# Kernel tuning notes

Hardware: AMD Instinct MI355X
Metric: run time of the kernel (lower is better)

The kernel has to match this reference:

```python
import jax, jax.numpy as jnp
import numpy as np

N_NODES = 100000
N_EDGES = 1250000
N_GRAPHS = 512
HIDDEN = 64
F_IN = 3
N_CLASSES = 5


def setup_inputs() -> dict:
    key = jax.random.key(0)
    ks = jax.random.split(key, 8)
    x = jax.random.normal(ks[0], (N_NODES, F_IN), dtype=jnp.float32)
    edge_index = jax.random.randint(ks[1], (2, N_EDGES), 0, N_NODES, dtype=jnp.int64)
    batch = jnp.sort(jax.random.randint(ks[2], (N_NODES,), 0, N_GRAPHS, dtype=jnp.int64))
    def glorot(k, shape):
        lim = (6.0 / (shape[0] + shape[1])) ** 0.5
        return jax.random.uniform(k, shape, jnp.float32, -lim, lim)
    return {
        "x": x,
        "edge_index": edge_index,
        "batch": batch,
        "W1": glorot(ks[3], (F_IN, HIDDEN)),
        "b1": jnp.zeros((HIDDEN,), jnp.float32),
        "W2": glorot(ks[4], (HIDDEN, HIDDEN)),
        "b2": jnp.zeros((HIDDEN,), jnp.float32),
        "Wl": glorot(ks[5], (HIDDEN, N_CLASSES)),
        "bl": jnp.zeros((N_CLASSES,), jnp.float32),
    }


def _gcn_conv(x, W, b, src, dst, deg_inv_sqrt):
    # GCNConv: x' = D^{-1/2} (A + I) D^{-1/2} X W + b  (self-loops added)
    h = x @ W                                   # [N, H]
    norm = deg_inv_sqrt[src] * deg_inv_sqrt[dst]  # per-edge scale
    agg = jax.ops.segment_sum(h[src] * norm[:, None], dst, num_segments=N_NODES)
    agg = agg + h * (deg_inv_sqrt * deg_inv_sqrt)[:, None]  # self-loop term
    return agg + b


def reference(x, edge_index, batch, W1, b1, W2, b2, Wl, bl):
    src, dst = edge_index[0], edge_index[1]
    # degree (with self-loop) on destination nodes, as in PyG GCNConv
    ones = jnp.ones((N_EDGES,), jnp.float32)
    deg = jax.ops.segment_sum(ones, dst, num_segments=N_NODES) + 1.0
    deg_inv_sqrt = 1.0 / jnp.sqrt(deg)

    h = jax.nn.relu(_gcn_conv(x, W1, b1, src, dst, deg_inv_sqrt))
    h = _gcn_conv(h, W2, b2, src, dst, deg_inv_sqrt)

    # global_mean_pool over graph ids
    sums = jax.ops.segment_sum(h, batch, num_segments=N_GRAPHS)
    cnts = jax.ops.segment_sum(jnp.ones((N_NODES,), jnp.float32), batch, num_segments=N_GRAPHS)
    pooled = sums / jnp.maximum(cnts, 1.0)[:, None]

    # dropout p=0.5 is identity in eval mode
    return pooled @ Wl + bl
```

## Files before the change

### kernel.cpp

```cpp
#include <hip/hip_runtime.h>
#include <hip/hip_bf16.h>

#define N_NODES   100000
#define N_EDGES   1250000
#define N_GRAPHS  512
#define HIDDEN    64
#define F_IN      3
#define N_CLASSES 5

#define BKT_SHIFT 8
#define BKT_NODES 256
#define N_BKT     ((N_NODES + BKT_NODES - 1) / BKT_NODES)
#define CAP       4096
#define EBLK      512
#define ECHUNK    ((N_EDGES + EBLK - 1) / EBLK)
#define SCT       512
#define NREP      8

__device__ __forceinline__ unsigned short f2bf(float f) {
    unsigned u = __float_as_uint(f);
    u += 0x7FFF + ((u >> 16) & 1);
    return (unsigned short)(u >> 16);
}

__global__ void k_scat(const int* __restrict__ src, const int* __restrict__ dst,
                       const float* __restrict__ W2, const float* __restrict__ Wl,
                       const float* __restrict__ b2, const float* __restrict__ bl,
                       const int* __restrict__ batch,
                       int* __restrict__ gcur, int* __restrict__ ebuf,
                       float* __restrict__ Wc, float* __restrict__ bc,
                       int* __restrict__ gstart) {
    int b = blockIdx.x;
    int tid = threadIdx.x;
    if (b >= EBLK) {
        int bb = b - EBLK;
        if (bb == 0) {
            for (int t = tid; t < HIDDEN * N_CLASSES + N_CLASSES; t += SCT) {
                if (t < HIDDEN * N_CLASSES) {
                    int k = t / N_CLASSES, c = t % N_CLASSES;
                    float acc = 0.0f;
#pragma unroll
                    for (int j = 0; j < HIDDEN; j++)
                        acc = fmaf(W2[k * HIDDEN + j], Wl[j * N_CLASSES + c], acc);
                    Wc[t] = acc;
                } else {
                    int c = t - HIDDEN * N_CLASSES;
                    float acc = bl[c];
#pragma unroll
                    for (int j = 0; j < HIDDEN; j++)
                        acc = fmaf(b2[j], Wl[j * N_CLASSES + c], acc);
                    bc[c] = acc;
                }
            }
            return;
        }
        int n = (bb - 1) * SCT + tid;
        if (n >= N_NODES) return;
        if (n == 0) {
            for (int g = 0; g <= batch[0]; g++) gstart[g] = 0;
        } else {
            int b0 = batch[n - 1], b1 = batch[n];
            for (int g = b0 + 1; g <= b1; g++) gstart[g] = n;
        }
        if (n == N_NODES - 1) {
            for (int g = batch[n] + 1; g <= N_GRAPHS; g++) gstart[g] = N_NODES;
        }
        return;
    }
    __shared__ int pk[ECHUNK];
    __shared__ unsigned short bkl[ECHUNK];
    __shared__ int spk[ECHUNK];
    __shared__ unsigned short sbk[ECHUNK];
    __shared__ int h[N_BKT];
    __shared__ int lsc[N_BKT];
    __shared__ int gb[N_BKT];
    __shared__ int cur[N_BKT];
    for (int i = tid; i < N_BKT; i += SCT) h[i] = 0;
    __syncthreads();
    int e0 = b * ECHUNK;
    int m = min(ECHUNK, N_EDGES - e0);
    for (int i = tid; i < m; i += SCT) {
        int s = src[e0 + i], d = dst[e0 + i];
        int bk = d >> BKT_SHIFT;
        pk[i] = (s << BKT_SHIFT) | (d & (BKT_NODES - 1));
        bkl[i] = (unsigned short)bk;
        atomicAdd(&h[bk], 1);
    }
    __syncthreads();
    if (tid < N_BKT) lsc[tid] = h[tid];
    __syncthreads();
    for (int off = 1; off < N_BKT; off <<= 1) {
        int t = 0;
        if (tid < N_BKT && tid >= off) t = lsc[tid - off];
        __syncthreads();
        if (tid < N_BKT) lsc[tid] += t;
        __syncthreads();
    }
    if (tid < N_BKT) {
        gb[tid] = atomicAdd(&gcur[tid], h[tid]);
        cur[tid] = lsc[tid] - h[tid];
    }
    __syncthreads();
    for (int i = tid; i < m; i += SCT) {
        int bk = bkl[i];
        int p = atomicAdd(&cur[bk], 1);
        spk[p] = pk[i];
        sbk[p] = (unsigned short)bk;
    }
    __syncthreads();
    for (int i = tid; i < m; i += SCT) {
        int bk = sbk[i];
        int gpos = gb[bk] + (i - (lsc[bk] - h[bk]));
        if (gpos < CAP)
            ebuf[bk * CAP + gpos] = spk[i];
    }
}

__global__ void k_bktfill(const int* __restrict__ ebuf, const int* __restrict__ gcur,
                          const float* __restrict__ x,
                          int* __restrict__ rowptr, int* __restrict__ deg,
                          float* __restrict__ dis, uint2* __restrict__ xs4,
                          int* __restrict__ elist) {
    __shared__ int eb_l[CAP];
    __shared__ int sorted_l[CAP];
    __shared__ int cnt_l[BKT_NODES];
    __shared__ int cur_l[BKT_NODES];
    __shared__ int ps[BKT_NODES];
    int b = blockIdx.x, tid = threadIdx.x;
    int n0 = b * BKT_NODES;
    int e0 = b * CAP;
    int cnt = min(gcur[b], CAP);
    if (tid < BKT_NODES) cnt_l[tid] = 0;
    __syncthreads();
    for (int i = tid; i < cnt; i += 1024) {
        int pe = ebuf[e0 + i];
        eb_l[i] = pe;
        atomicAdd(&cnt_l[pe & (BKT_NODES - 1)], 1);
    }
    __syncthreads();
    if (tid < BKT_NODES) ps[tid] = cnt_l[tid];
    __syncthreads();
    for (int off = 1; off < BKT_NODES; off <<= 1) {
        int t = 0;
        if (tid < BKT_NODES && tid >= off) t = ps[tid - off];
        __syncthreads();
        if (tid < BKT_NODES) ps[tid] += t;
        __syncthreads();
    }
    if (tid < BKT_NODES) {
        int node = n0 + tid;
        int excl = ps[tid] - cnt_l[tid];
        cur_l[tid] = excl;
        if (node < N_NODES) {
            rowptr[node] = e0 + excl;
            deg[node] = cnt_l[tid];
            float dv = rsqrtf((float)cnt_l[tid] + 1.0f);
            dis[node] = dv;
            float x0 = x[node * 3 + 0], x1 = x[node * 3 + 1], x2 = x[node * 3 + 2];
            xs4[node] = make_uint2((unsigned)f2bf(x0 * dv) |
                                   ((unsigned)f2bf(x1 * dv) << 16),
                                   (unsigned)f2bf(x2 * dv));
        }
    }
    __syncthreads();
    for (int i = tid; i < cnt; i += 1024) {
        int pe = eb_l[i];
        int pos = atomicAdd(&cur_l[pe & (BKT_NODES - 1)], 1);
        sorted_l[pos] = ((unsigned)pe) >> BKT_SHIFT;
    }
    __syncthreads();
    for (int i = tid; i < cnt; i += 1024)
        elist[e0 + i] = sorted_l[i];
}

__global__ void k_l1fused(const int* __restrict__ rp, const int* __restrict__ degA,
                          const int* __restrict__ elist,
                          const float* __restrict__ dis, const uint2* __restrict__ xs4,
                          const float* __restrict__ W1, const float* __restrict__ b1,
                          unsigned* __restrict__ h1b) {
    int w = threadIdx.x >> 6, lane = threadIdx.x & 63;
    int q4 = lane >> 4;
    int j  = lane & 15;
    int node = blockIdx.x * 16 + w * 4 + q4;
    int start = rp[node], dg = degA[node];
    float a0 = 0.f, a1 = 0.f, a2 = 0.f;
    for (int k = 0; k < dg; k += 32) {
        int ia = k + j, ib = k + 16 + j;
        bool aa = ia < dg, ab = ib < dg;
        int sa = elist[start + (aa ? ia : 0)];
        int sb = elist[start + (ab ? ib : 0)];
        uint2 ua = xs4[sa];
        uint2 ub = xs4[sb];
        float ma = aa ? 1.0f : 0.0f;
        float mb = ab ? 1.0f : 0.0f;
        a0 = fmaf(__uint_as_float(ua.x << 16), ma, a0);
        a1 = fmaf(__uint_as_float(ua.x & 0xFFFF0000u), ma, a1);
        a2 = fmaf(__uint_as_float(ua.y << 16), ma, a2);
        a0 = fmaf(__uint_as_float(ub.x << 16), mb, a0);
        a1 = fmaf(__uint_as_float(ub.x & 0xFFFF0000u), mb, a1);
        a2 = fmaf(__uint_as_float(ub.y << 16), mb, a2);
    }
#pragma unroll
    for (int off = 1; off < 16; off <<= 1) {
        a0 += __shfl_xor(a0, off);
        a1 += __shfl_xor(a1, off);
        a2 += __shfl_xor(a2, off);
    }
    uint2 un = xs4[node];
    float dn = dis[node];
    a0 = dn * (a0 + __uint_as_float(un.x << 16));
    a1 = dn * (a1 + __uint_as_float(un.x & 0xFFFF0000u));
    a2 = dn * (a2 + __uint_as_float(un.y << 16));
    float v[4];
#pragma unroll
    for (int i = 0; i < 4; i++) {
        int c = 4 * j + i;
        float t = a0 * W1[c] + a1 * W1[HIDDEN + c] + a2 * W1[2 * HIDDEN + c] + b1[c];
        v[i] = fmaxf(t, 0.0f) * dn;
    }
    unsigned w0 = (unsigned)f2bf(v[0]) | ((unsigned)f2bf(v[1]) << 16);
    unsigned w1 = (unsigned)f2bf(v[2]) | ((unsigned)f2bf(v[3]) << 16);
    *(uint2*)(h1b + (size_t)node * 32 + j * 2) = make_uint2(w0, w1);
}

__global__ void k_gatherpool(const int* __restrict__ rp, const int* __restrict__ degA,
                             const int* __restrict__ elist,
                             const float* __restrict__ dis,
                             const unsigned* __restrict__ h1b,
                             const int* __restrict__ batch,
                             float* __restrict__ gsum8) {
    __shared__ float acc_s[8][HIDDEN];
    __shared__ int gid[8];
    int w = threadIdx.x >> 6, lane = threadIdx.x & 63;
    int half = lane >> 5;
    int l32 = lane & 31;
    int node = blockIdx.x * 8 + w * 2 + half;
    int start = rp[node], dg = degA[node];
    int eg = l32 >> 3;
    int ch = lane & 7;
    float acc[8] = {0.f, 0.f, 0.f, 0.f, 0.f, 0.f, 0.f, 0.f};
    for (int k = 0; k < dg; k += 16) {
        int i0 = k + eg, i1 = k + 4 + eg, i2 = k + 8 + eg, i3 = k + 12 + eg;
        bool a0b = i0 < dg, a1b = i1 < dg, a2b = i2 < dg, a3b = i3 < dg;
        int s0 = elist[start + (a0b ? i0 : 0)];
        int s1 = elist[start + (a1b ? i1 : 0)];
        int s2 = elist[start + (a2b ? i2 : 0)];
        int s3 = elist[start + (a3b ? i3 : 0)];
        float m0 = a0b ? 1.0f : 0.0f;
        float m1 = a1b ? 1.0f : 0.0f;
        float m2 = a2b ? 1.0f : 0.0f;
        float m3 = a3b ? 1.0f : 0.0f;
        uint4 u0 = *(const uint4*)(h1b + (size_t)s0 * 32 + ch * 4);
        uint4 u1 = *(const uint4*)(h1b + (size_t)s1 * 32 + ch * 4);
        uint4 u2 = *(const uint4*)(h1b + (size_t)s2 * 32 + ch * 4);
        uint4 u3 = *(const uint4*)(h1b + (size_t)s3 * 32 + ch * 4);
        acc[0] = fmaf(__uint_as_float(u0.x << 16),          m0, acc[0]);
        acc[1] = fmaf(__uint_as_float(u0.x & 0xFFFF0000u),  m0, acc[1]);
        acc[2] = fmaf(__uint_as_float(u0.y << 16),          m0, acc[2]);
        acc[3] = fmaf(__uint_as_float(u0.y & 0xFFFF0000u),  m0, acc[3]);
        acc[4] = fmaf(__uint_as_float(u0.z << 16),          m0, acc[4]);
        acc[5] = fmaf(__uint_as_float(u0.z & 0xFFFF0000u),  m0, acc[5]);
        acc[6] = fmaf(__uint_as_float(u0.w << 16),          m0, acc[6]);
        acc[7] = fmaf(__uint_as_float(u0.w & 0xFFFF0000u),  m0, acc[7]);
        acc[0] = fmaf(__uint_as_float(u1.x << 16),          m1, acc[0]);
        acc[1] = fmaf(__uint_as_float(u1.x & 0xFFFF0000u),  m1, acc[1]);
        acc[2] = fmaf(__uint_as_float(u1.y << 16),          m1, acc[2]);
        acc[3] = fmaf(__uint_as_float(u1.y & 0xFFFF0000u),  m1, acc[3]);
        acc[4] = fmaf(__uint_as_float(u1.z << 16),          m1, acc[4]);
        acc[5] = fmaf(__uint_as_float(u1.z & 0xFFFF0000u),  m1, acc[5]);
        acc[6] = fmaf(__uint_as_float(u1.w << 16),          m1, acc[6]);
        acc[7] = fmaf(__uint_as_float(u1.w & 0xFFFF0000u),  m1, acc[7]);
        acc[0] = fmaf(__uint_as_float(u2.x << 16),          m2, acc[0]);
        acc[1] = fmaf(__uint_as_float(u2.x & 0xFFFF0000u),  m2, acc[1]);
        acc[2] = fmaf(__uint_as_float(u2.y << 16),          m2, acc[2]);
        acc[3] = fmaf(__uint_as_float(u2.y & 0xFFFF0000u),  m2, acc[3]);
        acc[4] = fmaf(__uint_as_float(u2.z << 16),          m2, acc[4]);
        acc[5] = fmaf(__uint_as_float(u2.z & 0xFFFF0000u),  m2, acc[5]);
        acc[6] = fmaf(__uint_as_float(u2.w << 16),          m2, acc[6]);
        acc[7] = fmaf(__uint_as_float(u2.w & 0xFFFF0000u),  m2, acc[7]);
        acc[0] = fmaf(__uint_as_float(u3.x << 16),          m3, acc[0]);
        acc[1] = fmaf(__uint_as_float(u3.x & 0xFFFF0000u),  m3, acc[1]);
        acc[2] = fmaf(__uint_as_float(u3.y << 16),          m3, acc[2]);
        acc[3] = fmaf(__uint_as_float(u3.y & 0xFFFF0000u),  m3, acc[3]);
        acc[4] = fmaf(__uint_as_float(u3.z << 16),          m3, acc[4]);
        acc[5] = fmaf(__uint_as_float(u3.z & 0xFFFF0000u),  m3, acc[5]);
        acc[6] = fmaf(__uint_as_float(u3.w << 16),          m3, acc[6]);
        acc[7] = fmaf(__uint_as_float(u3.w & 0xFFFF0000u),  m3, acc[7]);
    }
#pragma unroll
    for (int i = 0; i < 8; i++) {
        acc[i] += __shfl_xor(acc[i], 8);
        acc[i] += __shfl_xor(acc[i], 16);
    }
    if (l32 == 0) gid[w * 2 + half] = batch[node];
    if (l32 < 8) {
        float dn = dis[node];
        uint4 u = *(const uint4*)(h1b + (size_t)node * 32 + l32 * 4);
        float o[8];
        o[0] = dn * (acc[0] + __uint_as_float(u.x << 16));
        o[1] = dn * (acc[1] + __uint_as_float(u.x & 0xFFFF0000u));
        o[2] = dn * (acc[2] + __uint_as_float(u.y << 16));
        o[3] = dn * (acc[3] + __uint_as_float(u.y & 0xFFFF0000u));
        o[4] = dn * (acc[4] + __uint_as_float(u.z << 16));
        o[5] = dn * (acc[5] + __uint_as_float(u.z & 0xFFFF0000u));
        o[6] = dn * (acc[6] + __uint_as_float(u.w << 16));
        o[7] = dn * (acc[7] + __uint_as_float(u.w & 0xFFFF0000u));
        float* dst = &acc_s[w * 2 + half][l32 * 8];
        *(float4*)(dst)     = make_float4(o[0], o[1], o[2], o[3]);
        *(float4*)(dst + 4) = make_float4(o[4], o[5], o[6], o[7]);
    }
    __syncthreads();
    float* gs = gsum8 + (size_t)(blockIdx.x & (NREP - 1)) * (N_GRAPHS * HIDDEN);
    if (threadIdx.x < HIDDEN) {
        int t = threadIdx.x;
#pragma unroll
        for (int wv = 0; wv < 8; wv++) {
            int gw = gid[wv];
            bool first = true;
#pragma unroll
            for (int u = 0; u < wv; u++)
                if (gid[u] == gw) first = false;
            if (first) {
                float s = acc_s[wv][t];
#pragma unroll
                for (int u2 = wv + 1; u2 < 8; u2++)
                    if (gid[u2] == gw) s += acc_s[u2][t];
                atomicAdd(&gs[gw * HIDDEN + t], s);
            }
        }
    }
}

__global__ void k_head(const float* __restrict__ gsum8, const int* __restrict__ gstart,
                       const float* __restrict__ Wc, const float* __restrict__ bc,
                       float* __restrict__ out) {
    __shared__ float gl[HIDDEN];
    int g = blockIdx.x, t = threadIdx.x;
    float s = 0.0f;
#pragma unroll
    for (int r = 0; r < NREP; r++)
        s += gsum8[(size_t)r * (N_GRAPHS * HIDDEN) + g * HIDDEN + t];
    gl[t] = s;
    __syncthreads();
    if (t < N_CLASSES) {
        float cntf = fmaxf((float)(gstart[g + 1] - gstart[g]), 1.0f);
        float dot = 0.0f;
#pragma unroll
        for (int k = 0; k < HIDDEN; k++)
            dot = fmaf(gl[k], Wc[k * N_CLASSES + t], dot);
        out[g * N_CLASSES + t] = dot / cntf + bc[t];
    }
}

extern "C" void kernel_launch(void* const* d_in, const int* in_sizes, int n_in,
                              void* d_out, int out_size, void* d_ws, size_t ws_size,
                              hipStream_t stream) {
    const float* x     = (const float*)d_in[0];
    const int*   ei    = (const int*)  d_in[1];
    const int*   batch = (const int*)  d_in[2];
    const float* W1    = (const float*)d_in[3];
    const float* b1    = (const float*)d_in[4];
    const float* W2    = (const float*)d_in[5];
    const float* b2    = (const float*)d_in[6];
    const float* Wl    = (const float*)d_in[7];
    const float* bl    = (const float*)d_in[8];
    float* out = (float*)d_out;

    const int* src = ei;
    const int* dst = ei + N_EDGES;

    int*   gcur    = (int*)d_ws;
    float* gsum8   = (float*)(gcur + 512);
    int*   ebuf    = (int*)(gsum8 + NREP * N_GRAPHS * HIDDEN);
    int*   elist   = ebuf + N_BKT * CAP;
    int*   rp      = elist + N_BKT * CAP;
    int*   deg     = rp + N_NODES;
    float* dis     = (float*)(deg + N_NODES);
    uint2* xs4     = (uint2*)(dis + N_NODES);
    unsigned* h1b  = (unsigned*)(xs4 + N_NODES);
    int*   gstart  = (int*)(h1b + (size_t)N_NODES * 32);
    float* Wc      = (float*)(gstart + 516);
    float* bc      = Wc + HIDDEN * N_CLASSES;

    const int BS = 256;
    const int g_nodes_sct = (N_NODES + SCT - 1) / SCT;

    hipMemsetAsync(gcur, 0, (512 + NREP * N_GRAPHS * HIDDEN) * sizeof(int), stream);
    k_scat<<<EBLK + 1 + g_nodes_sct, SCT, 0, stream>>>(src, dst, W2, Wl, b2, bl, batch,
                                                       gcur, ebuf, Wc, bc, gstart);
    k_bktfill<<<N_BKT, 1024, 0, stream>>>(ebuf, gcur, x, rp, deg, dis, xs4, elist);

    k_l1fused<<<N_NODES / 16, BS, 0, stream>>>(rp, deg, elist, dis, xs4, W1, b1,
                                               h1b);

    k_gatherpool<<<N_NODES / 8, BS, 0, stream>>>(rp, deg, elist, dis, h1b,
                                                 batch, gsum8);

    k_head<<<N_GRAPHS, HIDDEN, 0, stream>>>(gsum8, gstart, Wc, bc, out);
}
```

Before: 143.8 us.

## Double edge-scatter blocks, vectorize edge loads, pack rowptr and degree into one word

```diff
diff --git a/kernel.cpp b/kernel.cpp
--- a/kernel.cpp
+++ b/kernel.cpp
@@ -12,8 +12,8 @@
 #define BKT_NODES 256
 #define N_BKT     ((N_NODES + BKT_NODES - 1) / BKT_NODES)
 #define CAP       4096
-#define EBLK      512
-#define ECHUNK    ((N_EDGES + EBLK - 1) / EBLK)
+#define EBLK      1024
+#define ECHUNK    ((((N_EDGES + EBLK - 1) / EBLK) + 1) & ~1)
 #define SCT       512
 #define NREP      8
 
@@ -79,12 +79,18 @@
     __syncthreads();
     int e0 = b * ECHUNK;
     int m = min(ECHUNK, N_EDGES - e0);
-    for (int i = tid; i < m; i += SCT) {
-        int s = src[e0 + i], d = dst[e0 + i];
-        int bk = d >> BKT_SHIFT;
-        pk[i] = (s << BKT_SHIFT) | (d & (BKT_NODES - 1));
-        bkl[i] = (unsigned short)bk;
-        atomicAdd(&h[bk], 1);
+    if (m < 0) m = 0;
+    for (int i = tid * 2; i < m; i += 2 * SCT) {
+        int2 s2 = *(const int2*)(src + e0 + i);
+        int2 d2 = *(const int2*)(dst + e0 + i);
+        int bk0 = d2.x >> BKT_SHIFT;
+        int bk1 = d2.y >> BKT_SHIFT;
+        pk[i]     = (s2.x << BKT_SHIFT) | (d2.x & (BKT_NODES - 1));
+        pk[i + 1] = (s2.y << BKT_SHIFT) | (d2.y & (BKT_NODES - 1));
+        bkl[i]     = (unsigned short)bk0;
+        bkl[i + 1] = (unsigned short)bk1;
+        atomicAdd(&h[bk0], 1);
+        atomicAdd(&h[bk1], 1);
     }
     __syncthreads();
     if (tid < N_BKT) lsc[tid] = h[tid];
@@ -118,7 +124,7 @@
 
 __global__ void k_bktfill(const int* __restrict__ ebuf, const int* __restrict__ gcur,
                           const float* __restrict__ x,
-                          int* __restrict__ rowptr, int* __restrict__ deg,
+                          int* __restrict__ rpd,
                           float* __restrict__ dis, uint2* __restrict__ xs4,
                           int* __restrict__ elist) {
     __shared__ int eb_l[CAP];
@@ -152,9 +158,9 @@
         int excl = ps[tid] - cnt_l[tid];
         cur_l[tid] = excl;
         if (node < N_NODES) {
-            rowptr[node] = e0 + excl;
-            deg[node] = cnt_l[tid];
-            float dv = rsqrtf((float)cnt_l[tid] + 1.0f);
+            int dgc = cnt_l[tid];
+            rpd[node] = ((e0 + excl) << 8) | min(dgc, 255);
+            float dv = rsqrtf((float)dgc + 1.0f);
             dis[node] = dv;
             float x0 = x[node * 3 + 0], x1 = x[node * 3 + 1], x2 = x[node * 3 + 2];
             xs4[node] = make_uint2((unsigned)f2bf(x0 * dv) |
@@ -173,7 +179,7 @@
         elist[e0 + i] = sorted_l[i];
 }
 
-__global__ void k_l1fused(const int* __restrict__ rp, const int* __restrict__ degA,
+__global__ void k_l1fused(const int* __restrict__ rpdA,
                           const int* __restrict__ elist,
                           const float* __restrict__ dis, const uint2* __restrict__ xs4,
                           const float* __restrict__ W1, const float* __restrict__ b1,
@@ -182,7 +188,9 @@
     int q4 = lane >> 4;
     int j  = lane & 15;
     int node = blockIdx.x * 16 + w * 4 + q4;
-    int start = rp[node], dg = degA[node];
+    int rv = rpdA[node];
+    int start = ((unsigned)rv) >> 8;
+    int dg = rv & 255;
     float a0 = 0.f, a1 = 0.f, a2 = 0.f;
     for (int k = 0; k < dg; k += 32) {
         int ia = k + j, ib = k + 16 + j;
@@ -223,7 +231,7 @@
     *(uint2*)(h1b + (size_t)node * 32 + j * 2) = make_uint2(w0, w1);
 }
 
-__global__ void k_gatherpool(const int* __restrict__ rp, const int* __restrict__ degA,
+__global__ void k_gatherpool(const int* __restrict__ rpdA,
                              const int* __restrict__ elist,
                              const float* __restrict__ dis,
                              const unsigned* __restrict__ h1b,
@@ -235,7 +243,9 @@
     int half = lane >> 5;
     int l32 = lane & 31;
     int node = blockIdx.x * 8 + w * 2 + half;
-    int start = rp[node], dg = degA[node];
+    int rv = rpdA[node];
+    int start = ((unsigned)rv) >> 8;
+    int dg = rv & 255;
     int eg = l32 >> 3;
     int ch = lane & 7;
     float acc[8] = {0.f, 0.f, 0.f, 0.f, 0.f, 0.f, 0.f, 0.f};
@@ -373,9 +383,8 @@
     float* gsum8   = (float*)(gcur + 512);
     int*   ebuf    = (int*)(gsum8 + NREP * N_GRAPHS * HIDDEN);
     int*   elist   = ebuf + N_BKT * CAP;
-    int*   rp      = elist + N_BKT * CAP;
-    int*   deg     = rp + N_NODES;
-    float* dis     = (float*)(deg + N_NODES);
+    int*   rpd     = elist + N_BKT * CAP;
+    float* dis     = (float*)(rpd + N_NODES);
     uint2* xs4     = (uint2*)(dis + N_NODES);
     unsigned* h1b  = (unsigned*)(xs4 + N_NODES);
     int*   gstart  = (int*)(h1b + (size_t)N_NODES * 32);
@@ -388,12 +397,11 @@
     hipMemsetAsync(gcur, 0, (512 + NREP * N_GRAPHS * HIDDEN) * sizeof(int), stream);
     k_scat<<<EBLK + 1 + g_nodes_sct, SCT, 0, stream>>>(src, dst, W2, Wl, b2, bl, batch,
                                                        gcur, ebuf, Wc, bc, gstart);
-    k_bktfill<<<N_BKT, 1024, 0, stream>>>(ebuf, gcur, x, rp, deg, dis, xs4, elist);
-
-    k_l1fused<<<N_NODES / 16, BS, 0, stream>>>(rp, deg, elist, dis, xs4, W1, b1,
-                                               h1b);
-
-    k_gatherpool<<<N_NODES / 8, BS, 0, stream>>>(rp, deg, elist, dis, h1b,
+    k_bktfill<<<N_BKT, 1024, 0, stream>>>(ebuf, gcur, x, rpd, dis, xs4, elist);
+
+    k_l1fused<<<N_NODES / 16, BS, 0, stream>>>(rpd, elist, dis, xs4, W1, b1, h1b);
+
+    k_gatherpool<<<N_NODES / 8, BS, 0, stream>>>(rpd, elist, dis, h1b,
                                                  batch, gsum8);
 
     k_head<<<N_GRAPHS, HIDDEN, 0, stream>>>(gsum8, gstart, Wc, bc, out);
```

Measured after the change: 150.8 us. 1.05x slower.
